# Optimization experiments

Measured on AMD Instinct MI355X. Metric: run time of the kernel, lower is better.

Reference implementation:

```python
import jax, jax.numpy as jnp
import numpy as np

EMBED_DIM = 1280
NUM_HEADS = 20
HEAD_DIM = EMBED_DIM // NUM_HEADS  # 64
TGT_LEN = 2048
BSZ = 2
SCALING = HEAD_DIM ** -0.5


def setup_inputs() -> dict:
    key = jax.random.key(0)
    ks = jax.random.split(key, 6)
    s = EMBED_DIM ** -0.5
    query = jax.random.normal(ks[0], (TGT_LEN, BSZ, EMBED_DIM), dtype=jnp.float32)
    Wq = jax.random.normal(ks[1], (EMBED_DIM, EMBED_DIM), dtype=jnp.float32) * s
    Wk = jax.random.normal(ks[2], (EMBED_DIM, EMBED_DIM), dtype=jnp.float32) * s
    Wv = jax.random.normal(ks[3], (EMBED_DIM, EMBED_DIM), dtype=jnp.float32) * s
    Wo = jax.random.normal(ks[4], (EMBED_DIM, EMBED_DIM), dtype=jnp.float32) * s
    bq = jnp.zeros((EMBED_DIM,), jnp.float32)
    bk = jnp.zeros((EMBED_DIM,), jnp.float32)
    bv = jnp.zeros((EMBED_DIM,), jnp.float32)
    bo = jnp.zeros((EMBED_DIM,), jnp.float32)
    # key_padding_mask: (bsz, src_len), True = padded; pad last 256 keys of batch 1
    kpm = np.zeros((BSZ, TGT_LEN), dtype=bool)
    kpm[1, -256:] = True
    key_padding_mask = jnp.asarray(kpm)
    return {"query": query, "key_padding_mask": key_padding_mask,
            "Wq": Wq, "bq": bq, "Wk": Wk, "bk": bk,
            "Wv": Wv, "bv": bv, "Wo": Wo, "bo": bo}


def _mha(query, key_padding_mask, Wq, bq, Wk, bk, Wv, bv, Wo, bo):
    T, B, E = query.shape
    H, D = NUM_HEADS, HEAD_DIM
    q = (query @ Wq + bq) * SCALING            # [T, B, E]
    k = query @ Wk + bk
    v = query @ Wv + bv
    # reshape to [B*H, T, D] as in the TF code
    q = q.reshape(T, B * H, D).transpose(1, 0, 2)
    k = k.reshape(T, B * H, D).transpose(1, 0, 2)
    v = v.reshape(T, B * H, D).transpose(1, 0, 2)
    attn_weights = jnp.einsum('bqd,bkd->bqk', q, k)   # [B*H, T, T]
    # key padding mask: (B, src_len), 1s excluded -> -inf
    aw = attn_weights.reshape(B, H, T, T)
    aw = jnp.where(key_padding_mask[:, None, None, :], -jnp.inf, aw)
    attn_weights_float = jax.nn.softmax(aw.astype(jnp.float32).reshape(B * H, T, T), axis=-1)
    attn_probs = attn_weights_float.astype(v.dtype)  # dropout rate 0.0 -> identity
    attn = jnp.einsum('bqk,bkd->bqd', attn_probs, v)  # [B*H, T, D]
    attn = attn.transpose(1, 0, 2).reshape(T, B, E)
    attn = attn @ Wo + bo
    # need_weights=True (default), need_head_weights=False -> mean over heads
    avg_weights = attn_weights_float.reshape(B, H, T, T).transpose(1, 0, 2, 3).mean(axis=0)
    return attn, avg_weights


def reference(query, key_padding_mask, Wq, bq, Wk, bk, Wv, bv, Wo, bo):
    return _mha(query, key_padding_mask, Wq, bq, Wk, bk, Wv, bv, Wo, bo)
```

## Files before the change

### kernel.cpp

```cpp
#include <hip/hip_runtime.h>

#define T_LEN 2048
#define BSZ   2
#define EMB   1280
#define NH    20
#define HD    64
#define NBH   (BSZ*NH)
#define NR    (T_LEN*BSZ)
#define QSCALE (0.125f * 1.4426950408889634f)

#define KPAD 68

typedef short bf16x8 __attribute__((ext_vector_type(8)));
typedef short bf16x4 __attribute__((ext_vector_type(4)));
typedef float f32x4  __attribute__((ext_vector_type(4)));

__device__ inline short f2bf(float f) {
    union { float f; unsigned u; } v; v.f = f;
    unsigned u = v.u + 0x7FFF + ((v.u >> 16) & 1);
    return (short)(u >> 16);
}

__device__ inline unsigned cvt_pk_bf16(float lo, float hi) {
    unsigned r;
    asm("v_cvt_pk_bf16_f32 %0, %1, %2" : "=v"(r) : "v"(lo), "v"(hi));
    return r;
}

__device__ inline void glds16(const short* g, short* l) {
    __builtin_amdgcn_global_load_lds(
        (const __attribute__((address_space(1))) void*)g,
        (__attribute__((address_space(3))) void*)l,
        16, 0, 0);
}

__global__ __launch_bounds__(256) void k_cvt_x(
    const float* __restrict__ X, short* __restrict__ Xb)
{
    size_t i0 = ((size_t)blockIdx.x*256 + threadIdx.x) * 8;
    float4 a = *(const float4*)(X + i0);
    float4 b = *(const float4*)(X + i0 + 4);
    bf16x8 r = { f2bf(a.x), f2bf(a.y), f2bf(a.z), f2bf(a.w),
                 f2bf(b.x), f2bf(b.y), f2bf(b.z), f2bf(b.w) };
    *(bf16x8*)(Xb + i0) = r;
}

__global__ __launch_bounds__(256) void k_cvt_wt(
    const float* __restrict__ Wq, const float* __restrict__ Wk,
    const float* __restrict__ Wv, const float* __restrict__ Wo,
    short* __restrict__ Wqt, short* __restrict__ Wkt,
    short* __restrict__ Wvt, short* __restrict__ Wot)
{
    const int z = blockIdx.z;
    const float* __restrict__ W = (z==0)?Wq:(z==1)?Wk:(z==2)?Wv:Wo;
    short* __restrict__ Wt      = (z==0)?Wqt:(z==1)?Wkt:(z==2)?Wvt:Wot;

    const int k0 = blockIdx.y * 32;
    const int n0 = blockIdx.x * 32;
    const int t  = threadIdx.x;

    __shared__ float Ls[32][33];
    {
        int row = t >> 3, col = (t & 7) * 4;
        *(float4*)&Ls[row][col] = *(const float4*)(W + (size_t)(k0+row)*EMB + n0 + col);
    }
    __syncthreads();
    {
        int n = t >> 3, k4 = (t & 7) * 4;
        bf16x4 r = { f2bf(Ls[k4+0][n]), f2bf(Ls[k4+1][n]),
                     f2bf(Ls[k4+2][n]), f2bf(Ls[k4+3][n]) };
        *(bf16x4*)(Wt + (size_t)(n0+n)*EMB + k0 + k4) = r;
    }
}

__global__ __launch_bounds__(256) void k_gemm_qkv(
    const short* __restrict__ Xb,
    const short* __restrict__ Wqt, const short* __restrict__ Wkt, const short* __restrict__ Wvt,
    const float* __restrict__ bq, const float* __restrict__ bk, const float* __restrict__ bv,
    short* __restrict__ Qb, short* __restrict__ Kb, short* __restrict__ Vt)
{
    const int which = blockIdx.z;
    const short* __restrict__ Wt   = (which==0) ? Wqt : (which==1) ? Wkt : Wvt;
    const float* __restrict__ bias = (which==0) ? bq  : (which==1) ? bk  : bv;
    const float scale = (which==0) ? QSCALE : 1.0f;

    const int bm = blockIdx.y * 128;
    const int bn = blockIdx.x * 128;
    const int t    = threadIdx.x;
    const int wave = t >> 6, lane = t & 63;
    const int l16  = lane & 15, quad = lane >> 4;
    const int wm   = (wave >> 1) * 64, wn = (wave & 1) * 64;

    __shared__ short As[128][64];
    __shared__ short Bs[128][64];

    const int srow   = lane >> 3;
    const int scolsw = (((lane & 7) ^ srow) & 7) * 8;
    const int rsw    = (l16 & 7) << 3;

    f32x4 acc[4][4] = {};

    for (int kt = 0; kt < EMB; kt += 64) {
        __syncthreads();
        const short* Ag = Xb + (size_t)bm*EMB + kt;
        const short* Bg = Wt + (size_t)bn*EMB + kt;
        #pragma unroll
        for (int c = 0; c < 4; ++c) {
            int seg = wave*4 + c;
            int grow = seg*8 + srow;
            glds16(Ag + (size_t)grow*EMB + scolsw, &As[seg*8][0]);
            glds16(Bg + (size_t)grow*EMB + scolsw, &Bs[seg*8][0]);
        }
        __syncthreads();
        #pragma unroll
        for (int ks = 0; ks < 64; ks += 32) {
            bf16x8 af[4], bfr[4];
            #pragma unroll
            for (int mi=0;mi<4;++mi) af[mi]  = *(const bf16x8*)&As[wm + mi*16 + l16][(ks + quad*8) ^ rsw];
            #pragma unroll
            for (int ni=0;ni<4;++ni) bfr[ni] = *(const bf16x8*)&Bs[wn + ni*16 + l16][(ks + quad*8) ^ rsw];
            #pragma unroll
            for (int mi=0;mi<4;++mi)
                #pragma unroll
                for (int ni=0;ni<4;++ni)
                    acc[mi][ni] = __builtin_amdgcn_mfma_f32_16x16x32_bf16(af[mi], bfr[ni], acc[mi][ni], 0,0,0);
        }
    }

    #pragma unroll
    for (int ni=0;ni<4;++ni) {
        int c = bn + wn + ni*16 + l16;
        float bval = bias[c];
        int h = c >> 6, d = c & 63;
        #pragma unroll
        for (int mi=0;mi<4;++mi) {
            #pragma unroll
            for (int j=0;j<4;++j) {
                int r = bm + wm + mi*16 + quad*4 + j;
                int tt = r >> 1, bb = r & 1;
                float val = (acc[mi][ni][j] + bval) * scale;
                if (which == 2)
                    Vt[((size_t)(bb*NH+h)*HD + d)*T_LEN + tt] = f2bf(val);
                else {
                    short* dst = (which==0) ? Qb : Kb;
                    dst[((size_t)(bb*NH+h)*T_LEN + tt)*HD + d] = f2bf(val);
                }
            }
        }
    }
}

__global__ __launch_bounds__(512) void k_pv(
    const short* __restrict__ Qb, const short* __restrict__ Kb, const short* __restrict__ Vt,
    const int* __restrict__ kpm,
    float* __restrict__ Linv,
    short* __restrict__ AttnMidb)
{
    int lin = blockIdx.y*gridDim.x + blockIdx.x;
    lin = (lin & 7) * 80 + (lin >> 3);
    const int qt = lin & 15;
    const int bh = lin >> 4;
    const int b  = bh / NH, h = bh % NH;
    const int t    = threadIdx.x;
    const int w    = t >> 6;
    const int lane = t & 63;
    const int l16  = lane & 15;
    const int quad = lane >> 4;
    const int q0   = qt*128 + w*16;

    __shared__ short Ks[2][64][KPAD];
    __shared__ short Vts[2][64][KPAD];
    __shared__ float MfL[2][64];
    __shared__ float Lsh[128];

    bf16x8 qf[2];
    #pragma unroll
    for (int ch=0;ch<2;++ch)
        qf[ch] = *(const bf16x8*)(Qb + ((size_t)bh*T_LEN + q0 + l16)*HD + ch*32 + quad*8);

    const int row0 = t >> 3, col8 = (t & 7) * 8;
    const short* Kgb = Kb + (size_t)bh*T_LEN*HD;
    const short* Vgb = Vt + (size_t)bh*HD*T_LEN;

    *(bf16x8*)&Ks[0][row0][col8]  = *(const bf16x8*)(Kgb + (size_t)row0*HD + col8);
    *(bf16x8*)&Vts[0][row0][col8] = *(const bf16x8*)(Vgb + (size_t)row0*T_LEN + col8);
    if (t < 64) MfL[0][t] = kpm[b*T_LEN + t] ? 0.f : 1.f;
    __syncthreads();

    f32x4 o[4] = {};
    float l = 0.f;
    int cur = 0;

    for (int kt = 0; kt < T_LEN; kt += 64) {
        const int ktn = kt + 64;
        const bool has_next = ktn < T_LEN;
        const int nxt = cur ^ 1;

        bf16x8 kr0, vr0;
        float mfn = 0.f;
        if (has_next) {
            kr0 = *(const bf16x8*)(Kgb + (size_t)(ktn + row0)*HD + col8);
            vr0 = *(const bf16x8*)(Vgb + (size_t)row0*T_LEN + ktn + col8);
            if (t < 64) mfn = kpm[b*T_LEN + ktn + t] ? 0.f : 1.f;
        }

        f32x4 s[4] = {};
        #pragma unroll
        for (int ch = 0; ch < 2; ++ch) {
            bf16x8 ka[4];
            #pragma unroll
            for (int mb=0;mb<4;++mb) ka[mb] = *(const bf16x8*)&Ks[cur][mb*16 + l16][ch*32 + quad*8];
            #pragma unroll
            for (int mb=0;mb<4;++mb)
                s[mb] = __builtin_amdgcn_mfma_f32_16x16x32_bf16(ka[mb], qf[ch], s[mb], 0,0,0);
        }

        unsigned pu[2][4];
        #pragma unroll
        for (int c = 0; c < 2; ++c) {
            #pragma unroll
            for (int mb2 = 0; mb2 < 2; ++mb2) {
                const int mb = c*2 + mb2;
                float4 mf = *(const float4*)&MfL[cur][mb*16 + quad*4];
                float p0 = __builtin_amdgcn_exp2f(s[mb][0]) * mf.x;
                float p1 = __builtin_amdgcn_exp2f(s[mb][1]) * mf.y;
                float p2 = __builtin_amdgcn_exp2f(s[mb][2]) * mf.z;
                float p3 = __builtin_amdgcn_exp2f(s[mb][3]) * mf.w;
                l += (p0 + p1) + (p2 + p3);
                pu[c][mb2*2+0] = cvt_pk_bf16(p0, p1);
                pu[c][mb2*2+1] = cvt_pk_bf16(p2, p3);
            }
        }

        if (has_next) {
            *(bf16x8*)&Ks[nxt][row0][col8]  = kr0;
            *(bf16x8*)&Vts[nxt][row0][col8] = vr0;
            if (t < 64) MfL[nxt][t] = mfn;
        }

        #pragma unroll
        for (int c = 0; c < 2; ++c) {
            bf16x8 vv[4];
            #pragma unroll
            for (int nb=0;nb<4;++nb) {
                bf16x4 va = *(const bf16x4*)&Vts[cur][nb*16 + l16][c*32 + quad*4];
                bf16x4 vb = *(const bf16x4*)&Vts[cur][nb*16 + l16][c*32 + 16 + quad*4];
                vv[nb] = (bf16x8){va[0],va[1],va[2],va[3], vb[0],vb[1],vb[2],vb[3]};
            }
            union { unsigned u[4]; bf16x8 v; } pa;
            pa.u[0]=pu[c][0]; pa.u[1]=pu[c][1];
            pa.u[2]=pu[c][2]; pa.u[3]=pu[c][3];
            #pragma unroll
            for (int nb=0;nb<4;++nb)
                o[nb] = __builtin_amdgcn_mfma_f32_16x16x32_bf16(pa.v, vv[nb], o[nb], 0,0,0);
        }

        __syncthreads();
        cur = nxt;
    }

    l += __shfl_xor(l, 16);
    l += __shfl_xor(l, 32);
    float linv = 1.0f / l;
    if (quad == 0) {
        Linv[(size_t)bh*T_LEN + q0 + l16] = linv;
        Lsh[w*16 + l16] = linv;
    }
    {
        float4 li = *(const float4*)&Lsh[w*16 + quad*4];
        float lr[4] = {li.x, li.y, li.z, li.w};
        #pragma unroll
        for (int r=0;r<4;++r) {
            int q = q0 + quad*4 + r;
            size_t base = ((size_t)q*BSZ + b)*EMB + h*HD;
            #pragma unroll
            for (int nb=0;nb<4;++nb)
                AttnMidb[base + nb*16 + l16] = f2bf(o[nb][r] * lr[r]);
        }
    }
}

__global__ __launch_bounds__(256) void k_meanw(
    const short* __restrict__ Qb, const short* __restrict__ Kb,
    const int* __restrict__ kpm,
    const float* __restrict__ Linv,
    float* __restrict__ avg)
{
    int lin = (blockIdx.z*gridDim.y + blockIdx.y)*gridDim.x + blockIdx.x;
    lin = (lin & 7) * 256 + (lin >> 3);
    const int kt = lin & 31;
    const int qt = (lin >> 5) & 31;
    const int b  = lin >> 10;

    const int t    = threadIdx.x;
    const int wave = t >> 6, lane = t & 63;
    const int l16  = lane & 15, quad = lane >> 4;

    __shared__ short Qs[2][64][KPAD];
    __shared__ short Ks[2][64][KPAD];
    __shared__ float Lish[2][64];
    __shared__ int   msk[64];

    const int srow = t >> 2;
    const int scol = (t & 3) * 16;

    const short* Qg0 = Qb + ((size_t)(b*NH)*T_LEN + qt*64)*HD;
    const short* Kg0 = Kb + ((size_t)(b*NH)*T_LEN + kt*64)*HD;
    const size_t hstride = (size_t)T_LEN*HD;

    if (t < 64) msk[t] = kpm[b*T_LEN + kt*64 + t];

    *(bf16x8*)&Qs[0][srow][scol]   = *(const bf16x8*)(Qg0 + (size_t)srow*HD + scol);
    *(bf16x8*)&Qs[0][srow][scol+8] = *(const bf16x8*)(Qg0 + (size_t)srow*HD + scol + 8);
    *(bf16x8*)&Ks[0][srow][scol]   = *(const bf16x8*)(Kg0 + (size_t)srow*HD + scol);
    *(bf16x8*)&Ks[0][srow][scol+8] = *(const bf16x8*)(Kg0 + (size_t)srow*HD + scol + 8);
    if (t < 64) Lish[0][t] = Linv[(size_t)(b*NH)*T_LEN + qt*64 + t];
    __syncthreads();

    f32x4 acc[4] = {};
    const int qrow_in = wave*16 + quad*4;
    int cur = 0;

    for (int h = 0; h < NH; ++h) {
        const int nxt = cur ^ 1;

        bf16x8 qr0, qr1, kr0, kr1;
        float lnx = 0.f;
        if (h+1 < NH) {
            const short* Qg = Qg0 + (size_t)(h+1)*hstride;
            const short* Kg = Kg0 + (size_t)(h+1)*hstride;
            qr0 = *(const bf16x8*)(Qg + (size_t)srow*HD + scol);
            qr1 = *(const bf16x8*)(Qg + (size_t)srow*HD + scol + 8);
            kr0 = *(const bf16x8*)(Kg + (size_t)srow*HD + scol);
            kr1 = *(const bf16x8*)(Kg + (size_t)srow*HD + scol + 8);
            if (t < 64) lnx = Linv[(size_t)(b*NH + h+1)*T_LEN + qt*64 + t];
        }

        bf16x8 aq0 = *(const bf16x8*)&Qs[cur][wave*16 + l16][quad*8];
        bf16x8 aq1 = *(const bf16x8*)&Qs[cur][wave*16 + l16][32 + quad*8];

        float lv[4];
        #pragma unroll
        for (int r = 0; r < 4; ++r)
            lv[r] = Lish[cur][qrow_in + r] * (1.0f/NH);

        #pragma unroll
        for (int nb = 0; nb < 4; ++nb) {
            bf16x8 bk0 = *(const bf16x8*)&Ks[cur][nb*16 + l16][quad*8];
            bf16x8 bk1 = *(const bf16x8*)&Ks[cur][nb*16 + l16][32 + quad*8];
            f32x4 s = {};
            s = __builtin_amdgcn_mfma_f32_16x16x32_bf16(aq0, bk0, s, 0,0,0);
            s = __builtin_amdgcn_mfma_f32_16x16x32_bf16(aq1, bk1, s, 0,0,0);
            const bool mk = msk[nb*16 + l16] != 0;
            #pragma unroll
            for (int r = 0; r < 4; ++r)
                acc[nb][r] += mk ? 0.f : __builtin_amdgcn_exp2f(s[r]) * lv[r];
        }

        if (h+1 < NH) {
            *(bf16x8*)&Qs[nxt][srow][scol]   = qr0;
            *(bf16x8*)&Qs[nxt][srow][scol+8] = qr1;
            *(bf16x8*)&Ks[nxt][srow][scol]   = kr0;
            *(bf16x8*)&Ks[nxt][srow][scol+8] = kr1;
            if (t < 64) Lish[nxt][t] = lnx;
        }
        __syncthreads();
        cur = nxt;
    }

    #pragma unroll
    for (int r = 0; r < 4; ++r) {
        int q = qt*64 + qrow_in + r;
        size_t base = ((size_t)b*T_LEN + q) * T_LEN + (size_t)kt*64;
        #pragma unroll
        for (int nb = 0; nb < 4; ++nb)
            avg[base + nb*16 + l16] = acc[nb][r];
    }
}

__global__ __launch_bounds__(256) void k_gemm_out(
    const short* __restrict__ Ab, const short* __restrict__ Wot,
    const float* __restrict__ bo, float* __restrict__ out)
{
    const int bm = blockIdx.y * 128;
    const int bn = blockIdx.x * 128;
    const int t    = threadIdx.x;
    const int wave = t >> 6, lane = t & 63;
    const int l16  = lane & 15, quad = lane >> 4;
    const int wm   = (wave >> 1) * 64, wn = (wave & 1) * 64;

    __shared__ short As[128][64];
    __shared__ short Bs[128][64];

    const int srow   = lane >> 3;
    const int scolsw = (((lane & 7) ^ srow) & 7) * 8;
    const int rsw    = (l16 & 7) << 3;

    f32x4 acc[4][4] = {};

    for (int kt = 0; kt < EMB; kt += 64) {
        __syncthreads();
        const short* Ag = Ab  + (size_t)bm*EMB + kt;
        const short* Bg = Wot + (size_t)bn*EMB + kt;
        #pragma unroll
        for (int c = 0; c < 4; ++c) {
            int seg = wave*4 + c;
            int grow = seg*8 + srow;
            glds16(Ag + (size_t)grow*EMB + scolsw, &As[seg*8][0]);
            glds16(Bg + (size_t)grow*EMB + scolsw, &Bs[seg*8][0]);
        }
        __syncthreads();
        #pragma unroll
        for (int ks = 0; ks < 64; ks += 32) {
            bf16x8 af[4], bfr[4];
            #pragma unroll
            for (int mi=0;mi<4;++mi) af[mi]  = *(const bf16x8*)&As[wm + mi*16 + l16][(ks + quad*8) ^ rsw];
            #pragma unroll
            for (int ni=0;ni<4;++ni) bfr[ni] = *(const bf16x8*)&Bs[wn + ni*16 + l16][(ks + quad*8) ^ rsw];
            #pragma unroll
            for (int mi=0;mi<4;++mi)
                #pragma unroll
                for (int ni=0;ni<4;++ni)
                    acc[mi][ni] = __builtin_amdgcn_mfma_f32_16x16x32_bf16(af[mi], bfr[ni], acc[mi][ni], 0,0,0);
        }
    }

    #pragma unroll
    for (int ni=0;ni<4;++ni) {
        int c = bn + wn + ni*16 + l16;
        float bval = bo[c];
        #pragma unroll
        for (int mi=0;mi<4;++mi) {
            #pragma unroll
            for (int j=0;j<4;++j) {
                int r = bm + wm + mi*16 + quad*4 + j;
                out[(size_t)r*EMB + c] = acc[mi][ni][j] + bval;
            }
        }
    }
}

extern "C" void kernel_launch(void* const* d_in, const int* in_sizes, int n_in,
                              void* d_out, int out_size, void* d_ws, size_t ws_size,
                              hipStream_t stream) {
    const float* X   = (const float*)d_in[0];
    const int*   kpm = (const int*)  d_in[1];
    const float* Wq  = (const float*)d_in[2];
    const float* bq  = (const float*)d_in[3];
    const float* Wk  = (const float*)d_in[4];
    const float* bk  = (const float*)d_in[5];
    const float* Wv  = (const float*)d_in[6];
    const float* bv  = (const float*)d_in[7];
    const float* Wo  = (const float*)d_in[8];
    const float* bo  = (const float*)d_in[9];

    float* out = (float*)d_out;
    float* ws  = (float*)d_ws;

    const size_t QKV = (size_t)NBH * T_LEN * HD;
    float* Linv = ws;
    short* Xb   = (short*)(Linv + (size_t)NBH * T_LEN);
    short* Wqt  = Xb  + (size_t)NR * EMB;
    short* Wkt  = Wqt + (size_t)EMB * EMB;
    short* Wvt  = Wkt + (size_t)EMB * EMB;
    short* Wot  = Wvt + (size_t)EMB * EMB;
    short* Qb   = Wot + (size_t)EMB * EMB;
    short* Kb   = Qb  + QKV;
    short* Vt   = Kb  + QKV;
    short* Amid = Vt  + QKV;

    float* attn_out = out;
    float* avg      = out + (size_t)T_LEN * BSZ * EMB;

    k_cvt_x   <<<dim3((NR*EMB)/(256*8)), 256, 0, stream>>>(X, Xb);
    k_cvt_wt  <<<dim3(EMB/32, EMB/32, 4), 256, 0, stream>>>(Wq, Wk, Wv, Wo, Wqt, Wkt, Wvt, Wot);
    k_gemm_qkv<<<dim3(EMB/128, NR/128, 3), 256, 0, stream>>>(Xb, Wqt, Wkt, Wvt, bq, bk, bv, Qb, Kb, Vt);
    k_pv      <<<dim3(T_LEN/128, NBH),   512, 0, stream>>>(Qb, Kb, Vt, kpm, Linv, Amid);
    k_meanw   <<<dim3(T_LEN/64, T_LEN/64, BSZ), 256, 0, stream>>>(Qb, Kb, kpm, Linv, avg);
    k_gemm_out<<<dim3(EMB/128, NR/128),  256, 0, stream>>>(Amid, Wot, bo, attn_out);
}
```

Before: 341.4 us.

## Double per-wave query rows in attention kernel and swizzle GEMM block order

The PV attention kernel now runs with 256 threads per block, and each wave handles 32 query rows (two 16-row MFMA tiles) instead of 16. Each K/V fragment read from shared memory therefore feeds twice as many MFMAs. The V tile is stored in a permuted layout so the PV operand can be read with one 8-wide LDS load instead of two 4-wide loads plus a repack. Both GEMM kernels remap block indices so neighbouring blocks share row and column stripes, aiming at better L2 reuse. The trade-off is higher register use per thread and fewer waves per block to hide latency.

```diff
diff --git a/kernel.cpp b/kernel.cpp
--- a/kernel.cpp
+++ b/kernel.cpp
@@ -79,13 +79,19 @@
     const float* __restrict__ bq, const float* __restrict__ bk, const float* __restrict__ bv,
     short* __restrict__ Qb, short* __restrict__ Kb, short* __restrict__ Vt)
 {
-    const int which = blockIdx.z;
+    int orig = (blockIdx.z*gridDim.y + blockIdx.y)*gridDim.x + blockIdx.x;
+    int wp = (orig & 7)*120 + (orig >> 3);
+    const int bm2    = wp & 1;
+    const int bnn    = (wp >> 1) % 10;
+    const int stripe = (wp / 20) & 15;
+    const int which  = wp / 320;
+
     const short* __restrict__ Wt   = (which==0) ? Wqt : (which==1) ? Wkt : Wvt;
     const float* __restrict__ bias = (which==0) ? bq  : (which==1) ? bk  : bv;
     const float scale = (which==0) ? QSCALE : 1.0f;
 
-    const int bm = blockIdx.y * 128;
-    const int bn = blockIdx.x * 128;
+    const int bm = (stripe*2 + bm2) * 128;
+    const int bn = bnn * 128;
     const int t    = threadIdx.x;
     const int wave = t >> 6, lane = t & 63;
     const int l16  = lane & 15, quad = lane >> 4;
@@ -150,7 +156,7 @@
     }
 }
 
-__global__ __launch_bounds__(512) void k_pv(
+__global__ __launch_bounds__(256) void k_pv(
     const short* __restrict__ Qb, const short* __restrict__ Kb, const short* __restrict__ Vt,
     const int* __restrict__ kpm,
     float* __restrict__ Linv,
@@ -166,29 +172,44 @@
     const int lane = t & 63;
     const int l16  = lane & 15;
     const int quad = lane >> 4;
-    const int q0   = qt*128 + w*16;
+    const int q0   = qt*128 + w*32;
 
     __shared__ short Ks[2][64][KPAD];
     __shared__ short Vts[2][64][KPAD];
     __shared__ float MfL[2][64];
     __shared__ float Lsh[128];
 
-    bf16x8 qf[2];
-    #pragma unroll
-    for (int ch=0;ch<2;++ch)
-        qf[ch] = *(const bf16x8*)(Qb + ((size_t)bh*T_LEN + q0 + l16)*HD + ch*32 + quad*8);
-
-    const int row0 = t >> 3, col8 = (t & 7) * 8;
+    bf16x8 qf[2][2];
+    #pragma unroll
+    for (int mi=0;mi<2;++mi)
+        #pragma unroll
+        for (int ch=0;ch<2;++ch)
+            qf[mi][ch] = *(const bf16x8*)(Qb + ((size_t)bh*T_LEN + q0 + mi*16 + l16)*HD + ch*32 + quad*8);
+
+    const int row0 = t >> 3;
+    const int col8 = (t & 7) * 8;
+    const int cc = col8 >> 5, aa = (col8 >> 3) & 3;
+    const int vb = cc*32 + (((aa & 1) << 4) | ((aa >> 1) << 2));
+
     const short* Kgb = Kb + (size_t)bh*T_LEN*HD;
     const short* Vgb = Vt + (size_t)bh*HD*T_LEN;
 
-    *(bf16x8*)&Ks[0][row0][col8]  = *(const bf16x8*)(Kgb + (size_t)row0*HD + col8);
-    *(bf16x8*)&Vts[0][row0][col8] = *(const bf16x8*)(Vgb + (size_t)row0*T_LEN + col8);
+    #pragma unroll
+    for (int c2 = 0; c2 < 2; ++c2) {
+        int r = row0 + c2*32;
+        bf16x8 kv = *(const bf16x8*)(Kgb + (size_t)r*HD + col8);
+        bf16x8 vv = *(const bf16x8*)(Vgb + (size_t)r*T_LEN + col8);
+        *(bf16x8*)&Ks[0][r][col8] = kv;
+        bf16x4 vlo = {vv[0],vv[1],vv[2],vv[3]};
+        bf16x4 vhi = {vv[4],vv[5],vv[6],vv[7]};
+        *(bf16x4*)&Vts[0][r][vb]     = vlo;
+        *(bf16x4*)&Vts[0][r][vb + 8] = vhi;
+    }
     if (t < 64) MfL[0][t] = kpm[b*T_LEN + t] ? 0.f : 1.f;
     __syncthreads();
 
-    f32x4 o[4] = {};
-    float l = 0.f;
+    f32x4 o[2][4] = {};
+    float l[2] = {0.f, 0.f};
     int cur = 0;
 
     for (int kt = 0; kt < T_LEN; kt += 64) {
@@ -196,15 +217,19 @@
         const bool has_next = ktn < T_LEN;
         const int nxt = cur ^ 1;
 
-        bf16x8 kr0, vr0;
+        bf16x8 kr[2], vr[2];
         float mfn = 0.f;
         if (has_next) {
-            kr0 = *(const bf16x8*)(Kgb + (size_t)(ktn + row0)*HD + col8);
-            vr0 = *(const bf16x8*)(Vgb + (size_t)row0*T_LEN + ktn + col8);
+            #pragma unroll
+            for (int c2 = 0; c2 < 2; ++c2) {
+                int r = row0 + c2*32;
+                kr[c2] = *(const bf16x8*)(Kgb + (size_t)(ktn + r)*HD + col8);
+                vr[c2] = *(const bf16x8*)(Vgb + (size_t)r*T_LEN + ktn + col8);
+            }
             if (t < 64) mfn = kpm[b*T_LEN + ktn + t] ? 0.f : 1.f;
         }
 
-        f32x4 s[4] = {};
+        f32x4 s[4][2] = {};
         #pragma unroll
         for (int ch = 0; ch < 2; ++ch) {
             bf16x8 ka[4];
@@ -212,29 +237,41 @@
             for (int mb=0;mb<4;++mb) ka[mb] = *(const bf16x8*)&Ks[cur][mb*16 + l16][ch*32 + quad*8];
             #pragma unroll
             for (int mb=0;mb<4;++mb)
-                s[mb] = __builtin_amdgcn_mfma_f32_16x16x32_bf16(ka[mb], qf[ch], s[mb], 0,0,0);
-        }
-
-        unsigned pu[2][4];
+                #pragma unroll
+                for (int mi=0;mi<2;++mi)
+                    s[mb][mi] = __builtin_amdgcn_mfma_f32_16x16x32_bf16(ka[mb], qf[mi][ch], s[mb][mi], 0,0,0);
+        }
+
+        unsigned pu[2][2][4];
         #pragma unroll
         for (int c = 0; c < 2; ++c) {
             #pragma unroll
             for (int mb2 = 0; mb2 < 2; ++mb2) {
                 const int mb = c*2 + mb2;
                 float4 mf = *(const float4*)&MfL[cur][mb*16 + quad*4];
-                float p0 = __builtin_amdgcn_exp2f(s[mb][0]) * mf.x;
-                float p1 = __builtin_amdgcn_exp2f(s[mb][1]) * mf.y;
-                float p2 = __builtin_amdgcn_exp2f(s[mb][2]) * mf.z;
-                float p3 = __builtin_amdgcn_exp2f(s[mb][3]) * mf.w;
-                l += (p0 + p1) + (p2 + p3);
-                pu[c][mb2*2+0] = cvt_pk_bf16(p0, p1);
-                pu[c][mb2*2+1] = cvt_pk_bf16(p2, p3);
+                #pragma unroll
+                for (int mi = 0; mi < 2; ++mi) {
+                    float p0 = __builtin_amdgcn_exp2f(s[mb][mi][0]) * mf.x;
+                    float p1 = __builtin_amdgcn_exp2f(s[mb][mi][1]) * mf.y;
+                    float p2 = __builtin_amdgcn_exp2f(s[mb][mi][2]) * mf.z;
+                    float p3 = __builtin_amdgcn_exp2f(s[mb][mi][3]) * mf.w;
+                    l[mi] += (p0 + p1) + (p2 + p3);
+                    pu[c][mi][mb2*2+0] = cvt_pk_bf16(p0, p1);
+                    pu[c][mi][mb2*2+1] = cvt_pk_bf16(p2, p3);
+                }
             }
         }
 
         if (has_next) {
-            *(bf16x8*)&Ks[nxt][row0][col8]  = kr0;
-            *(bf16x8*)&Vts[nxt][row0][col8] = vr0;
+            #pragma unroll
+            for (int c2 = 0; c2 < 2; ++c2) {
+                int r = row0 + c2*32;
+                *(bf16x8*)&Ks[nxt][r][col8] = kr[c2];
+                bf16x4 vlo = {vr[c2][0],vr[c2][1],vr[c2][2],vr[c2][3]};
+                bf16x4 vhi = {vr[c2][4],vr[c2][5],vr[c2][6],vr[c2][7]};
+                *(bf16x4*)&Vts[nxt][r][vb]     = vlo;
+                *(bf16x4*)&Vts[nxt][r][vb + 8] = vhi;
+            }
             if (t < 64) MfL[nxt][t] = mfn;
         }
 
@@ -242,40 +279,44 @@
         for (int c = 0; c < 2; ++c) {
             bf16x8 vv[4];
             #pragma unroll
-            for (int nb=0;nb<4;++nb) {
-                bf16x4 va = *(const bf16x4*)&Vts[cur][nb*16 + l16][c*32 + quad*4];
-                bf16x4 vb = *(const bf16x4*)&Vts[cur][nb*16 + l16][c*32 + 16 + quad*4];
-                vv[nb] = (bf16x8){va[0],va[1],va[2],va[3], vb[0],vb[1],vb[2],vb[3]};
+            for (int nb=0;nb<4;++nb)
+                vv[nb] = *(const bf16x8*)&Vts[cur][nb*16 + l16][c*32 + quad*8];
+            #pragma unroll
+            for (int mi=0;mi<2;++mi) {
+                union { unsigned u[4]; bf16x8 v; } pa;
+                pa.u[0]=pu[c][mi][0]; pa.u[1]=pu[c][mi][1];
+                pa.u[2]=pu[c][mi][2]; pa.u[3]=pu[c][mi][3];
+                #pragma unroll
+                for (int nb=0;nb<4;++nb)
+                    o[mi][nb] = __builtin_amdgcn_mfma_f32_16x16x32_bf16(pa.v, vv[nb], o[mi][nb], 0,0,0);
             }
-            union { unsigned u[4]; bf16x8 v; } pa;
-            pa.u[0]=pu[c][0]; pa.u[1]=pu[c][1];
-            pa.u[2]=pu[c][2]; pa.u[3]=pu[c][3];
-            #pragma unroll
-            for (int nb=0;nb<4;++nb)
-                o[nb] = __builtin_amdgcn_mfma_f32_16x16x32_bf16(pa.v, vv[nb], o[nb], 0,0,0);
         }
 
         __syncthreads();
         cur = nxt;
     }
 
-    l += __shfl_xor(l, 16);
-    l += __shfl_xor(l, 32);
-    float linv = 1.0f / l;
-    if (quad == 0) {
-        Linv[(size_t)bh*T_LEN + q0 + l16] = linv;
-        Lsh[w*16 + l16] = linv;
-    }
-    {
-        float4 li = *(const float4*)&Lsh[w*16 + quad*4];
+    #pragma unroll
+    for (int mi=0;mi<2;++mi) {
+        l[mi] += __shfl_xor(l[mi], 16);
+        l[mi] += __shfl_xor(l[mi], 32);
+        float linv = 1.0f / l[mi];
+        if (quad == 0) {
+            Linv[(size_t)bh*T_LEN + q0 + mi*16 + l16] = linv;
+            Lsh[w*32 + mi*16 + l16] = linv;
+        }
+    }
+    #pragma unroll
+    for (int mi=0;mi<2;++mi) {
+        float4 li = *(const float4*)&Lsh[w*32 + mi*16 + quad*4];
         float lr[4] = {li.x, li.y, li.z, li.w};
         #pragma unroll
         for (int r=0;r<4;++r) {
-            int q = q0 + quad*4 + r;
+            int q = q0 + mi*16 + quad*4 + r;
             size_t base = ((size_t)q*BSZ + b)*EMB + h*HD;
             #pragma unroll
             for (int nb=0;nb<4;++nb)
-                AttnMidb[base + nb*16 + l16] = f2bf(o[nb][r] * lr[r]);
+                AttnMidb[base + nb*16 + l16] = f2bf(o[mi][nb][r] * lr[r]);
         }
     }
 }
@@ -382,8 +423,14 @@
     const short* __restrict__ Ab, const short* __restrict__ Wot,
     const float* __restrict__ bo, float* __restrict__ out)
 {
-    const int bm = blockIdx.y * 128;
-    const int bn = blockIdx.x * 128;
+    int orig = blockIdx.y*gridDim.x + blockIdx.x;
+    int wp = (orig & 7)*40 + (orig >> 3);
+    const int bm2    = wp & 1;
+    const int bnn    = (wp >> 1) % 10;
+    const int stripe = wp / 20;
+
+    const int bm = (stripe*2 + bm2) * 128;
+    const int bn = bnn * 128;
     const int t    = threadIdx.x;
     const int wave = t >> 6, lane = t & 63;
     const int l16  = lane & 15, quad = lane >> 4;
@@ -475,7 +522,7 @@
     k_cvt_x   <<<dim3((NR*EMB)/(256*8)), 256, 0, stream>>>(X, Xb);
     k_cvt_wt  <<<dim3(EMB/32, EMB/32, 4), 256, 0, stream>>>(Wq, Wk, Wv, Wo, Wqt, Wkt, Wvt, Wot);
     k_gemm_qkv<<<dim3(EMB/128, NR/128, 3), 256, 0, stream>>>(Xb, Wqt, Wkt, Wvt, bq, bk, bv, Qb, Kb, Vt);
-    k_pv      <<<dim3(T_LEN/128, NBH),   512, 0, stream>>>(Qb, Kb, Vt, kpm, Linv, Amid);
+    k_pv      <<<dim3(T_LEN/128, NBH),   256, 0, stream>>>(Qb, Kb, Vt, kpm, Linv, Amid);
     k_meanw   <<<dim3(T_LEN/64, T_LEN/64, BSZ), 256, 0, stream>>>(Qb, Kb, kpm, Linv, avg);
     k_gemm_out<<<dim3(EMB/128, NR/128),  256, 0, stream>>>(Amid, Wot, bo, attn_out);
 }
```

After: 351.1 us. 2.9% more time.

## Use direct global-to-LDS loads with swizzle, skip mask multiply, remap GEMM blocks

Applied to the files above, without the earlier changes.

The PV attention kernel now fills its K/V tiles with direct global-to-LDS loads (glds16) into an unpadded, XOR-swizzled layout instead of staging through registers into a padded layout. It also records a per-tile flag so tiles with no padded keys skip the mask multiply. Both projection GEMMs remap block indices so the eight XCDs each work on contiguous stripes sharing the same A rows and W tiles, to improve L2 locality. The swizzle must match the MFMA read addressing exactly, and the extra flag load adds a branch per tile.

```diff
diff --git a/kernel.cpp b/kernel.cpp
--- a/kernel.cpp
+++ b/kernel.cpp
@@ -79,13 +79,19 @@
     const float* __restrict__ bq, const float* __restrict__ bk, const float* __restrict__ bv,
     short* __restrict__ Qb, short* __restrict__ Kb, short* __restrict__ Vt)
 {
-    const int which = blockIdx.z;
+    int orig = (blockIdx.z*gridDim.y + blockIdx.y)*gridDim.x + blockIdx.x;
+    int wp = (orig & 7)*120 + (orig >> 3);
+    const int bm2    = wp & 1;
+    const int bnn    = (wp >> 1) % 10;
+    const int stripe = (wp / 20) & 15;
+    const int which  = wp / 320;
+
     const short* __restrict__ Wt   = (which==0) ? Wqt : (which==1) ? Wkt : Wvt;
     const float* __restrict__ bias = (which==0) ? bq  : (which==1) ? bk  : bv;
     const float scale = (which==0) ? QSCALE : 1.0f;
 
-    const int bm = blockIdx.y * 128;
-    const int bn = blockIdx.x * 128;
+    const int bm = (stripe*2 + bm2) * 128;
+    const int bn = bnn * 128;
     const int t    = threadIdx.x;
     const int wave = t >> 6, lane = t & 63;
     const int l16  = lane & 15, quad = lane >> 4;
@@ -168,9 +174,10 @@
     const int quad = lane >> 4;
     const int q0   = qt*128 + w*16;
 
-    __shared__ short Ks[2][64][KPAD];
-    __shared__ short Vts[2][64][KPAD];
+    __shared__ short Ks[2][64][64];
+    __shared__ short Vts[2][64][64];
     __shared__ float MfL[2][64];
+    __shared__ int   Mflag[2];
     __shared__ float Lsh[128];
 
     bf16x8 qf[2];
@@ -178,13 +185,20 @@
     for (int ch=0;ch<2;++ch)
         qf[ch] = *(const bf16x8*)(Qb + ((size_t)bh*T_LEN + q0 + l16)*HD + ch*32 + quad*8);
 
-    const int row0 = t >> 3, col8 = (t & 7) * 8;
+    const int srow = lane >> 3;
+    const int csw  = ((lane & 7) ^ srow) * 8;
+    const int rsw  = (l16 & 7) << 3;
     const short* Kgb = Kb + (size_t)bh*T_LEN*HD;
     const short* Vgb = Vt + (size_t)bh*HD*T_LEN;
 
-    *(bf16x8*)&Ks[0][row0][col8]  = *(const bf16x8*)(Kgb + (size_t)row0*HD + col8);
-    *(bf16x8*)&Vts[0][row0][col8] = *(const bf16x8*)(Vgb + (size_t)row0*T_LEN + col8);
-    if (t < 64) MfL[0][t] = kpm[b*T_LEN + t] ? 0.f : 1.f;
+    glds16(Kgb + (size_t)(w*8 + srow)*HD + csw,   &Ks[0][w*8][0]);
+    glds16(Vgb + (size_t)(w*8 + srow)*T_LEN + csw, &Vts[0][w*8][0]);
+    if (t < 64) {
+        float m0 = kpm[b*T_LEN + t] ? 0.f : 1.f;
+        MfL[0][t] = m0;
+        int fl = __any(m0 != 1.0f);
+        if (t == 0) Mflag[0] = fl;
+    }
     __syncthreads();
 
     f32x4 o[4] = {};
@@ -196,12 +210,9 @@
         const bool has_next = ktn < T_LEN;
         const int nxt = cur ^ 1;
 
-        bf16x8 kr0, vr0;
-        float mfn = 0.f;
         if (has_next) {
-            kr0 = *(const bf16x8*)(Kgb + (size_t)(ktn + row0)*HD + col8);
-            vr0 = *(const bf16x8*)(Vgb + (size_t)row0*T_LEN + ktn + col8);
-            if (t < 64) mfn = kpm[b*T_LEN + ktn + t] ? 0.f : 1.f;
+            glds16(Kgb + (size_t)(ktn + w*8 + srow)*HD + csw,   &Ks[nxt][w*8][0]);
+            glds16(Vgb + (size_t)(w*8 + srow)*T_LEN + ktn + csw, &Vts[nxt][w*8][0]);
         }
 
         f32x4 s[4] = {};
@@ -209,33 +220,52 @@
         for (int ch = 0; ch < 2; ++ch) {
             bf16x8 ka[4];
             #pragma unroll
-            for (int mb=0;mb<4;++mb) ka[mb] = *(const bf16x8*)&Ks[cur][mb*16 + l16][ch*32 + quad*8];
+            for (int mb=0;mb<4;++mb)
+                ka[mb] = *(const bf16x8*)&Ks[cur][mb*16 + l16][(ch*32 + quad*8) ^ rsw];
             #pragma unroll
             for (int mb=0;mb<4;++mb)
                 s[mb] = __builtin_amdgcn_mfma_f32_16x16x32_bf16(ka[mb], qf[ch], s[mb], 0,0,0);
         }
 
         unsigned pu[2][4];
-        #pragma unroll
-        for (int c = 0; c < 2; ++c) {
-            #pragma unroll
-            for (int mb2 = 0; mb2 < 2; ++mb2) {
-                const int mb = c*2 + mb2;
-                float4 mf = *(const float4*)&MfL[cur][mb*16 + quad*4];
-                float p0 = __builtin_amdgcn_exp2f(s[mb][0]) * mf.x;
-                float p1 = __builtin_amdgcn_exp2f(s[mb][1]) * mf.y;
-                float p2 = __builtin_amdgcn_exp2f(s[mb][2]) * mf.z;
-                float p3 = __builtin_amdgcn_exp2f(s[mb][3]) * mf.w;
-                l += (p0 + p1) + (p2 + p3);
-                pu[c][mb2*2+0] = cvt_pk_bf16(p0, p1);
-                pu[c][mb2*2+1] = cvt_pk_bf16(p2, p3);
+        if (Mflag[cur]) {
+            #pragma unroll
+            for (int c = 0; c < 2; ++c) {
+                #pragma unroll
+                for (int mb2 = 0; mb2 < 2; ++mb2) {
+                    const int mb = c*2 + mb2;
+                    float4 mf = *(const float4*)&MfL[cur][mb*16 + quad*4];
+                    float p0 = __builtin_amdgcn_exp2f(s[mb][0]) * mf.x;
+                    float p1 = __builtin_amdgcn_exp2f(s[mb][1]) * mf.y;
+                    float p2 = __builtin_amdgcn_exp2f(s[mb][2]) * mf.z;
+                    float p3 = __builtin_amdgcn_exp2f(s[mb][3]) * mf.w;
+                    l += (p0 + p1) + (p2 + p3);
+                    pu[c][mb2*2+0] = cvt_pk_bf16(p0, p1);
+                    pu[c][mb2*2+1] = cvt_pk_bf16(p2, p3);
+                }
             }
-        }
-
-        if (has_next) {
-            *(bf16x8*)&Ks[nxt][row0][col8]  = kr0;
-            *(bf16x8*)&Vts[nxt][row0][col8] = vr0;
-            if (t < 64) MfL[nxt][t] = mfn;
+        } else {
+            #pragma unroll
+            for (int c = 0; c < 2; ++c) {
+                #pragma unroll
+                for (int mb2 = 0; mb2 < 2; ++mb2) {
+                    const int mb = c*2 + mb2;
+                    float p0 = __builtin_amdgcn_exp2f(s[mb][0]);
+                    float p1 = __builtin_amdgcn_exp2f(s[mb][1]);
+                    float p2 = __builtin_amdgcn_exp2f(s[mb][2]);
+                    float p3 = __builtin_amdgcn_exp2f(s[mb][3]);
+                    l += (p0 + p1) + (p2 + p3);
+                    pu[c][mb2*2+0] = cvt_pk_bf16(p0, p1);
+                    pu[c][mb2*2+1] = cvt_pk_bf16(p2, p3);
+                }
+            }
+        }
+
+        if (has_next && t < 64) {
+            float mfn = kpm[b*T_LEN + ktn + t] ? 0.f : 1.f;
+            MfL[nxt][t] = mfn;
+            int fl = __any(mfn != 1.0f);
+            if (t == 0) Mflag[nxt] = fl;
         }
 
         #pragma unroll
@@ -243,8 +273,10 @@
             bf16x8 vv[4];
             #pragma unroll
             for (int nb=0;nb<4;++nb) {
-                bf16x4 va = *(const bf16x4*)&Vts[cur][nb*16 + l16][c*32 + quad*4];
-                bf16x4 vb = *(const bf16x4*)&Vts[cur][nb*16 + l16][c*32 + 16 + quad*4];
+                int c1 = (((c*4 + (quad>>1))     ^ (l16 & 7)) << 3) + (quad & 1)*4;
+                int c2 = (((c*4 + (quad>>1) + 2) ^ (l16 & 7)) << 3) + (quad & 1)*4;
+                bf16x4 va = *(const bf16x4*)&Vts[cur][nb*16 + l16][c1];
+                bf16x4 vb = *(const bf16x4*)&Vts[cur][nb*16 + l16][c2];
                 vv[nb] = (bf16x8){va[0],va[1],va[2],va[3], vb[0],vb[1],vb[2],vb[3]};
             }
             union { unsigned u[4]; bf16x8 v; } pa;
@@ -382,8 +414,14 @@
     const short* __restrict__ Ab, const short* __restrict__ Wot,
     const float* __restrict__ bo, float* __restrict__ out)
 {
-    const int bm = blockIdx.y * 128;
-    const int bn = blockIdx.x * 128;
+    int orig = blockIdx.y*gridDim.x + blockIdx.x;
+    int wp = (orig & 7)*40 + (orig >> 3);
+    const int bm2    = wp & 1;
+    const int bnn    = (wp >> 1) % 10;
+    const int stripe = wp / 20;
+
+    const int bm = (stripe*2 + bm2) * 128;
+    const int bn = bnn * 128;
     const int t    = threadIdx.x;
     const int wave = t >> 6, lane = t & 63;
     const int l16  = lane & 15, quad = lane >> 4;
```

New measurement: 360.4 us. 5.6% more time.

## Split PV head dim across two blocks and remap GEMM block order for XCD locality

Applied to the files above, without the earlier changes.

The attention PV kernel now launches twice as many blocks, each computing half of the 64-wide head dimension. Each half recomputes the full QK^T scores and softmax numerators, so QK work is duplicated in exchange for more blocks to fill the CUs. Both GEMM kernels also remap linear block IDs across the 8 XCDs so that neighbouring row and column tiles share L2. The changes target load imbalance and low occupancy in the PV stage, and cache reuse in the GEMMs.

```diff
diff --git a/kernel.cpp b/kernel.cpp
--- a/kernel.cpp
+++ b/kernel.cpp
@@ -79,13 +79,19 @@
     const float* __restrict__ bq, const float* __restrict__ bk, const float* __restrict__ bv,
     short* __restrict__ Qb, short* __restrict__ Kb, short* __restrict__ Vt)
 {
-    const int which = blockIdx.z;
+    int orig = (blockIdx.z*gridDim.y + blockIdx.y)*gridDim.x + blockIdx.x;
+    int wp = (orig & 7)*120 + (orig >> 3);
+    const int bm2    = wp & 1;
+    const int bnn    = (wp >> 1) % 10;
+    const int stripe = (wp / 20) & 15;
+    const int which  = wp / 320;
+
     const short* __restrict__ Wt   = (which==0) ? Wqt : (which==1) ? Wkt : Wvt;
     const float* __restrict__ bias = (which==0) ? bq  : (which==1) ? bk  : bv;
     const float scale = (which==0) ? QSCALE : 1.0f;
 
-    const int bm = blockIdx.y * 128;
-    const int bn = blockIdx.x * 128;
+    const int bm = (stripe*2 + bm2) * 128;
+    const int bn = bnn * 128;
     const int t    = threadIdx.x;
     const int wave = t >> 6, lane = t & 63;
     const int l16  = lane & 15, quad = lane >> 4;
@@ -156,10 +162,11 @@
     float* __restrict__ Linv,
     short* __restrict__ AttnMidb)
 {
-    int lin = blockIdx.y*gridDim.x + blockIdx.x;
-    lin = (lin & 7) * 80 + (lin >> 3);
+    int lin = blockIdx.y*32 + blockIdx.x;
+    lin = (lin & 7) * 160 + (lin >> 3);
     const int qt = lin & 15;
-    const int bh = lin >> 4;
+    const int dh = (lin >> 4) & 1;
+    const int bh = lin >> 5;
     const int b  = bh / NH, h = bh % NH;
     const int t    = threadIdx.x;
     const int w    = t >> 6;
@@ -169,7 +176,7 @@
     const int q0   = qt*128 + w*16;
 
     __shared__ short Ks[2][64][KPAD];
-    __shared__ short Vts[2][64][KPAD];
+    __shared__ short Vts[2][32][KPAD];
     __shared__ float MfL[2][64];
     __shared__ float Lsh[128];
 
@@ -180,14 +187,15 @@
 
     const int row0 = t >> 3, col8 = (t & 7) * 8;
     const short* Kgb = Kb + (size_t)bh*T_LEN*HD;
-    const short* Vgb = Vt + (size_t)bh*HD*T_LEN;
+    const short* Vgb = Vt + ((size_t)bh*HD + dh*32)*T_LEN;
 
     *(bf16x8*)&Ks[0][row0][col8]  = *(const bf16x8*)(Kgb + (size_t)row0*HD + col8);
-    *(bf16x8*)&Vts[0][row0][col8] = *(const bf16x8*)(Vgb + (size_t)row0*T_LEN + col8);
+    if (t < 256)
+        *(bf16x8*)&Vts[0][row0][col8] = *(const bf16x8*)(Vgb + (size_t)row0*T_LEN + col8);
     if (t < 64) MfL[0][t] = kpm[b*T_LEN + t] ? 0.f : 1.f;
     __syncthreads();
 
-    f32x4 o[4] = {};
+    f32x4 o[2] = {};
     float l = 0.f;
     int cur = 0;
 
@@ -200,7 +208,8 @@
         float mfn = 0.f;
         if (has_next) {
             kr0 = *(const bf16x8*)(Kgb + (size_t)(ktn + row0)*HD + col8);
-            vr0 = *(const bf16x8*)(Vgb + (size_t)row0*T_LEN + ktn + col8);
+            if (t < 256)
+                vr0 = *(const bf16x8*)(Vgb + (size_t)row0*T_LEN + ktn + col8);
             if (t < 64) mfn = kpm[b*T_LEN + ktn + t] ? 0.f : 1.f;
         }
 
@@ -234,15 +243,16 @@
 
         if (has_next) {
             *(bf16x8*)&Ks[nxt][row0][col8]  = kr0;
-            *(bf16x8*)&Vts[nxt][row0][col8] = vr0;
+            if (t < 256)
+                *(bf16x8*)&Vts[nxt][row0][col8] = vr0;
             if (t < 64) MfL[nxt][t] = mfn;
         }
 
         #pragma unroll
         for (int c = 0; c < 2; ++c) {
-            bf16x8 vv[4];
-            #pragma unroll
-            for (int nb=0;nb<4;++nb) {
+            bf16x8 vv[2];
+            #pragma unroll
+            for (int nb=0;nb<2;++nb) {
                 bf16x4 va = *(const bf16x4*)&Vts[cur][nb*16 + l16][c*32 + quad*4];
                 bf16x4 vb = *(const bf16x4*)&Vts[cur][nb*16 + l16][c*32 + 16 + quad*4];
                 vv[nb] = (bf16x8){va[0],va[1],va[2],va[3], vb[0],vb[1],vb[2],vb[3]};
@@ -251,7 +261,7 @@
             pa.u[0]=pu[c][0]; pa.u[1]=pu[c][1];
             pa.u[2]=pu[c][2]; pa.u[3]=pu[c][3];
             #pragma unroll
-            for (int nb=0;nb<4;++nb)
+            for (int nb=0;nb<2;++nb)
                 o[nb] = __builtin_amdgcn_mfma_f32_16x16x32_bf16(pa.v, vv[nb], o[nb], 0,0,0);
         }
 
@@ -263,7 +273,7 @@
     l += __shfl_xor(l, 32);
     float linv = 1.0f / l;
     if (quad == 0) {
-        Linv[(size_t)bh*T_LEN + q0 + l16] = linv;
+        if (dh == 0) Linv[(size_t)bh*T_LEN + q0 + l16] = linv;
         Lsh[w*16 + l16] = linv;
     }
     {
@@ -272,9 +282,9 @@
         #pragma unroll
         for (int r=0;r<4;++r) {
             int q = q0 + quad*4 + r;
-            size_t base = ((size_t)q*BSZ + b)*EMB + h*HD;
-            #pragma unroll
-            for (int nb=0;nb<4;++nb)
+            size_t base = ((size_t)q*BSZ + b)*EMB + h*HD + dh*32;
+            #pragma unroll
+            for (int nb=0;nb<2;++nb)
                 AttnMidb[base + nb*16 + l16] = f2bf(o[nb][r] * lr[r]);
         }
     }
@@ -382,8 +392,14 @@
     const short* __restrict__ Ab, const short* __restrict__ Wot,
     const float* __restrict__ bo, float* __restrict__ out)
 {
-    const int bm = blockIdx.y * 128;
-    const int bn = blockIdx.x * 128;
+    int orig = blockIdx.y*gridDim.x + blockIdx.x;
+    int wp = (orig & 7)*40 + (orig >> 3);
+    const int bm2    = wp & 1;
+    const int bnn    = (wp >> 1) % 10;
+    const int stripe = wp / 20;
+
+    const int bm = (stripe*2 + bm2) * 128;
+    const int bn = bnn * 128;
     const int t    = threadIdx.x;
     const int wave = t >> 6, lane = t & 63;
     const int l16  = lane & 15, quad = lane >> 4;
@@ -475,7 +491,7 @@
     k_cvt_x   <<<dim3((NR*EMB)/(256*8)), 256, 0, stream>>>(X, Xb);
     k_cvt_wt  <<<dim3(EMB/32, EMB/32, 4), 256, 0, stream>>>(Wq, Wk, Wv, Wo, Wqt, Wkt, Wvt, Wot);
     k_gemm_qkv<<<dim3(EMB/128, NR/128, 3), 256, 0, stream>>>(Xb, Wqt, Wkt, Wvt, bq, bk, bv, Qb, Kb, Vt);
-    k_pv      <<<dim3(T_LEN/128, NBH),   512, 0, stream>>>(Qb, Kb, Vt, kpm, Linv, Amid);
+    k_pv      <<<dim3(32, NBH),          512, 0, stream>>>(Qb, Kb, Vt, kpm, Linv, Amid);
     k_meanw   <<<dim3(T_LEN/64, T_LEN/64, BSZ), 256, 0, stream>>>(Qb, Kb, kpm, Linv, avg);
     k_gemm_out<<<dim3(EMB/128, NR/128),  256, 0, stream>>>(Amid, Wot, bo, attn_out);
 }
```

Measured after the change: 365.7 us. 7.1% more time.
